# Optimization experiments

Hardware: AMD Instinct MI355X
Metric: run time of the kernel (lower is better)

## Reference

```python
import jax, jax.numpy as jnp
import numpy as np

B, L, N, H, D, TOPK = 32, 720, 512, 16, 64, 8
TEMP = 1.0


def setup_inputs() -> dict:
    key = jax.random.key(0)
    ks = jax.random.split(key, 18)
    s = lambda k, shp, fan: jax.random.normal(k, shp, jnp.float32) / np.sqrt(fan)
    return {
        'x': jax.random.normal(ks[0], (B, L, N), jnp.float32),
        'var_embed': s(ks[1], (N, H), H),
        'Wq': s(ks[2], (H, H), H), 'bq': jnp.zeros((H,), jnp.float32),
        'Wk': s(ks[3], (H, H), H), 'bk': jnp.zeros((H,), jnp.float32),
        'Wscore': s(ks[4], (N, 1), N), 'bscore': jnp.zeros((1,), jnp.float32),
        'Wc1': s(ks[5], (N, D), N), 'bc1': jnp.zeros((D,), jnp.float32),
        'Wc2': s(ks[6], (D, D), D), 'bc2': jnp.zeros((D,), jnp.float32),
        'Wcn': s(ks[7], (D, N), D), 'bcn': jnp.zeros((N,), jnp.float32),
        'Wg': s(ks[8], (2 * N, N), 2 * N), 'bg': jnp.zeros((N,), jnp.float32),
        'Wf': s(ks[9], (N, N), N), 'bf': jnp.zeros((N,), jnp.float32),
        'gamma': jnp.ones((N,), jnp.float32), 'beta': jnp.zeros((N,), jnp.float32),
    }


def _forward(x, var_embed, Wq, bq, Wk, bk, Wscore, bscore, Wc1, bc1, Wc2, bc2,
             Wcn, bcn, Wg, bg, Wf, bf, gamma, beta):
    # --- SparseVariableRouter (eval mode: no gumbel noise) ---
    Q = var_embed @ Wq + bq          # [N,H]
    K = var_embed @ Wk + bk          # [N,H]
    sim = Q @ K.T                    # [N,N] (identical across batch in torch)
    eye = jnp.eye(N, dtype=bool)
    sim = jnp.where(eye, -1e9, sim)
    topk_vals, topk_idx = jax.lax.top_k(sim, TOPK)      # [N,k]
    w = jax.nn.softmax(topk_vals / TEMP, axis=-1)        # [N,k]
    x_perm = jnp.transpose(x, (0, 2, 1))                 # [B,N,L]
    neighbors = x_perm[:, topk_idx, :]                   # [B,N,k,L] gather
    ring_out = jnp.einsum('bnkl,nk->bln', neighbors, w)  # [B,L,N]
    # --- center path ---
    attn = jax.nn.softmax(x @ Wscore + bscore, axis=1)   # [B,L,1] softmax over L
    center_raw = jnp.sum(x * attn, axis=1)               # [B,N]
    c = jax.nn.gelu(center_raw @ Wc1 + bc1, approximate=False)
    c = jax.nn.gelu(c @ Wc2 + bc2, approximate=False)
    center = c @ Wcn + bcn                               # [B,N]
    center_b = jnp.broadcast_to(center[:, None, :], (x.shape[0], x.shape[1], N))
    # --- gated fusion + residual LN ---
    gate = jax.nn.sigmoid(jnp.concatenate([ring_out, center_b], axis=-1) @ Wg + bg)
    fused = gate * ring_out + (1.0 - gate) * center_b
    fused = fused @ Wf + bf
    h = fused + x
    mu = jnp.mean(h, axis=-1, keepdims=True)
    var = jnp.var(h, axis=-1, keepdims=True)
    return (h - mu) * jax.lax.rsqrt(var + 1e-5) * gamma + beta


def reference(x, var_embed, Wq, bq, Wk, bk, Wscore, bscore, Wc1, bc1, Wc2, bc2,
              Wcn, bcn, Wg, bg, Wf, bf, gamma, beta):
    return _forward(x, var_embed, Wq, bq, Wk, bk, Wscore, bscore, Wc1, bc1,
                    Wc2, bc2, Wcn, bcn, Wg, bg, Wf, bf, gamma, beta)
```

## Files before the change

### kernel.cpp

```cpp
#include <hip/hip_runtime.h>
#include <hip/hip_bf16.h>
#include <math.h>

#define B_ 32
#define L_ 720
#define N_ 512
#define H_ 16
#define D_ 64
#define TOPK_ 8
#define M_ (B_ * L_)
#define RPB 8
#define CRCH 16
#define CRL (L_ / CRCH)
#define OROWS 64

typedef __bf16 bf16x8 __attribute__((ext_vector_type(8)));
typedef float f32x16 __attribute__((ext_vector_type(16)));

__device__ __forceinline__ void async_cp16(const __hip_bfloat16* g, __hip_bfloat16* l) {
    __builtin_amdgcn_global_load_lds(
        (const __attribute__((address_space(1))) void*)g,
        (__attribute__((address_space(3))) void*)l, 16, 0, 0);
}

__device__ __forceinline__ bf16x8 frag_ld(const __hip_bfloat16* base, int row, int j0) {
    return *(const bf16x8*)(base + row * 64 + (((j0) ^ (row & 7)) << 3));
}

__device__ __forceinline__ f32x16 fzero16() {
    f32x16 z;
    #pragma unroll
    for (int e = 0; e < 16; ++e) z[e] = 0.f;
    return z;
}

__global__ __launch_bounds__(512) void qk_kernel(
    const float* __restrict__ ve,
    const float* __restrict__ Wq, const float* __restrict__ bq,
    const float* __restrict__ Wk, const float* __restrict__ bk,
    float* __restrict__ Qm, float* __restrict__ Km)
{
    const int g = blockIdx.x * 512 + threadIdx.x;
    const int j = g >> 4, h = g & 15;
    const float* vr = ve + j * H_;
    float q = bq[h], k = bk[h];
    #pragma unroll
    for (int m = 0; m < H_; ++m) {
        const float v = vr[m];
        q += v * Wq[m * H_ + h];
        k += v * Wk[m * H_ + h];
    }
    Qm[g] = q;
    Km[g] = k;
}

__global__ __launch_bounds__(64) void topk_kernel(
    const float* __restrict__ Qm, const float* __restrict__ Km,
    float* __restrict__ w_out, int* __restrict__ idx_out)
{
    const int n = blockIdx.x;
    const int lane = threadIdx.x;

    float4 q0, q1, q2, q3;
    {
        const float4* qr = (const float4*)(Qm + n * H_);
        q0 = qr[0]; q1 = qr[1]; q2 = qr[2]; q3 = qr[3];
    }

    float sv[8]; int si[8];
    #pragma unroll
    for (int c = 0; c < 8; ++c) {
        const int j = c * 64 + lane;
        const float4* kr = (const float4*)(Km + j * H_);
        float4 k0 = kr[0], k1 = kr[1], k2 = kr[2], k3 = kr[3];
        float s = q0.x * k0.x + q0.y * k0.y + q0.z * k0.z + q0.w * k0.w
                + q1.x * k1.x + q1.y * k1.y + q1.z * k1.z + q1.w * k1.w
                + q2.x * k2.x + q2.y * k2.y + q2.z * k2.z + q2.w * k2.w
                + q3.x * k3.x + q3.y * k3.y + q3.z * k3.z + q3.w * k3.w;
        sv[c] = (j == n) ? -1e9f : s;
        si[c] = j;
    }

    float keepv[TOPK_]; int keepi[TOPK_];
    #pragma unroll
    for (int k = 0; k < TOPK_; ++k) {
        float bv = sv[0]; int bi = si[0]; int bslot = 0;
        #pragma unroll
        for (int c = 1; c < 8; ++c)
            if (sv[c] > bv || (sv[c] == bv && si[c] < bi)) { bv = sv[c]; bi = si[c]; bslot = c; }
        float v = bv; int i = bi;
        #pragma unroll
        for (int off = 32; off > 0; off >>= 1) {
            float v2 = __shfl_xor(v, off);
            int   i2 = __shfl_xor(i, off);
            if (v2 > v || (v2 == v && i2 < i)) { v = v2; i = i2; }
        }
        keepv[k] = v; keepi[k] = i;
        if (i == bi) sv[bslot] = -INFINITY;
    }

    if (lane == 0) {
        float vmax = keepv[0];
        float ev[TOPK_], esum = 0.f;
        #pragma unroll
        for (int k = 0; k < TOPK_; k++) { ev[k] = expf(keepv[k] - vmax); esum += ev[k]; }
        float inv = 1.f / esum;
        #pragma unroll
        for (int k = 0; k < TOPK_; k++) {
            w_out[n * TOPK_ + k] = ev[k] * inv;
            idx_out[n * TOPK_ + k] = keepi[k];
        }
    }
}

__global__ __launch_bounds__(512) void ring_kernel(
    const float* __restrict__ x, const float* __restrict__ w,
    const int* __restrict__ idx,
    const float* __restrict__ Wscore, const float* __restrict__ bscore,
    __hip_bfloat16* __restrict__ ring, float* __restrict__ s)
{
    __shared__ float xs[RPB][N_];
    __shared__ float wsh[N_ * TOPK_];
    __shared__ int   ish[N_ * TOPK_];
    const int t = threadIdx.x;
    const int row0 = blockIdx.x * RPB;

    for (int i = t; i < N_ * TOPK_; i += 512) { wsh[i] = w[i]; ish[i] = idx[i]; }
    {
        const float4* xg = (const float4*)(x + (size_t)row0 * N_);
        float4* xsf = (float4*)&xs[0][0];
        xsf[t] = xg[t];
        xsf[t + 512] = xg[t + 512];
    }
    __syncthreads();

    {
        const int wv = t >> 6, lane = t & 63;
        float sa = 0.f;
        #pragma unroll
        for (int i = 0; i < 8; ++i) sa += xs[wv][lane + i * 64] * Wscore[lane + i * 64];
        for (int off = 32; off > 0; off >>= 1) sa += __shfl_down(sa, off);
        if (lane == 0) s[row0 + wv] = sa + bscore[0];
    }

    float wr[TOPK_]; int ir[TOPK_];
    #pragma unroll
    for (int k = 0; k < TOPK_; ++k) { wr[k] = wsh[t * TOPK_ + k]; ir[k] = ish[t * TOPK_ + k]; }
    #pragma unroll
    for (int r = 0; r < RPB; ++r) {
        float acc = 0.f;
        #pragma unroll
        for (int k = 0; k < TOPK_; ++k) acc += wr[k] * xs[r][ir[k]];
        ring[(size_t)(row0 + r) * N_ + t] = __float2bfloat16(acc);
    }
}

__global__ __launch_bounds__(256) void attn_softmax_kernel(float* __restrict__ s)
{
    const int b = blockIdx.x;
    const int t = threadIdx.x;
    float* row = s + (size_t)b * L_;

    __shared__ float sm[4];
    __shared__ float sm2[4];

    float lmax = -1e30f;
    for (int l = t; l < L_; l += 256) lmax = fmaxf(lmax, row[l]);
    for (int off = 32; off > 0; off >>= 1) lmax = fmaxf(lmax, __shfl_down(lmax, off));
    if ((t & 63) == 0) sm[t >> 6] = lmax;
    __syncthreads();
    float gmax = fmaxf(fmaxf(sm[0], sm[1]), fmaxf(sm[2], sm[3]));

    float lsum = 0.f;
    for (int l = t; l < L_; l += 256) {
        float e = expf(row[l] - gmax);
        row[l] = e;
        lsum += e;
    }
    for (int off = 32; off > 0; off >>= 1) lsum += __shfl_down(lsum, off);
    if ((t & 63) == 0) sm2[t >> 6] = lsum;
    __syncthreads();
    float inv = 1.f / (sm2[0] + sm2[1] + sm2[2] + sm2[3]);
    for (int l = t; l < L_; l += 256) row[l] *= inv;
}

__global__ __launch_bounds__(512) void center_raw_kernel(
    const float* __restrict__ x, const float* __restrict__ attn,
    float* __restrict__ craw_p)
{
    const int b = blockIdx.x >> 4;
    const int c = blockIdx.x & 15;
    const int n = threadIdx.x;
    __shared__ float ash[CRL];
    const int l0 = c * CRL;
    if (n < CRL) ash[n] = attn[b * L_ + l0 + n];
    __syncthreads();
    const float* xb = x + ((size_t)b * L_ + l0) * N_;
    float acc = 0.f;
    #pragma unroll 3
    for (int l = 0; l < CRL; l++) acc += ash[l] * xb[(size_t)l * N_ + n];
    craw_p[(size_t)(b * CRCH + c) * N_ + n] = acc;
}

__device__ __forceinline__ float gelu_exact(float v) {
    return 0.5f * v * (1.0f + erff(v * 0.70710678118654752440f));
}

__global__ __launch_bounds__(512) void center_mlp_kernel(
    const float* __restrict__ craw_p,
    const float* __restrict__ Wc1, const float* __restrict__ bc1,
    const float* __restrict__ Wc2, const float* __restrict__ bc2,
    const float* __restrict__ Wcn, const float* __restrict__ bcn,
    float* __restrict__ center)
{
    const int b = blockIdx.x;
    const int t = threadIdx.x;
    const int col = t & 63;
    const int seg = t >> 6;
    __shared__ float cr[N_];
    __shared__ float psum[8][D_];
    __shared__ float h1[D_];
    __shared__ float h2[D_];

    {
        float acc = 0.f;
        #pragma unroll
        for (int c = 0; c < CRCH; ++c) acc += craw_p[(size_t)(b * CRCH + c) * N_ + t];
        cr[t] = acc;
    }
    __syncthreads();
    {
        float p = 0.f;
        #pragma unroll 8
        for (int m = seg * 64; m < seg * 64 + 64; ++m) p += cr[m] * Wc1[m * D_ + col];
        psum[seg][col] = p;
    }
    __syncthreads();
    if (t < D_) {
        float acc = bc1[t];
        #pragma unroll
        for (int s2 = 0; s2 < 8; ++s2) acc += psum[s2][t];
        h1[t] = gelu_exact(acc);
    }
    __syncthreads();
    if (t < D_) {
        float acc = bc2[t];
        #pragma unroll 8
        for (int j = 0; j < D_; j++) acc += h1[j] * Wc2[j * D_ + t];
        h2[t] = gelu_exact(acc);
    }
    __syncthreads();
    {
        float acc = bcn[t];
        #pragma unroll 8
        for (int j = 0; j < D_; j++) acc += h2[j] * Wcn[j * N_ + t];
        center[b * N_ + t] = acc;
    }
}

__global__ __launch_bounds__(512) void cg_kernel(
    const float* __restrict__ center, const float* __restrict__ Wg,
    const float* __restrict__ bg, float* __restrict__ cg)
{
    const int nc = blockIdx.x;
    const int b  = blockIdx.y;
    const int t  = threadIdx.x;
    const int col = nc * 64 + (t & 63);
    const int seg = t >> 6;
    __shared__ float cs[N_];
    __shared__ float psum[8][64];

    cs[t] = center[b * N_ + t];
    __syncthreads();
    {
        float p = 0.f;
        const float* wp = Wg + (size_t)(N_ + seg * 64) * N_ + col;
        #pragma unroll 8
        for (int m = 0; m < 64; ++m) { p += cs[seg * 64 + m] * wp[0]; wp += N_; }
        psum[seg][t & 63] = p;
    }
    __syncthreads();
    if (t < 64) {
        float acc = bg[nc * 64 + t];
        #pragma unroll
        for (int s2 = 0; s2 < 8; ++s2) acc += psum[s2][t];
        cg[b * N_ + nc * 64 + t] = acc;
    }
}

__global__ __launch_bounds__(256) void convert_kernel(
    const float* __restrict__ Wg, const float* __restrict__ Wf,
    __hip_bfloat16* __restrict__ WgT, __hip_bfloat16* __restrict__ WfT)
{
    const int n = blockIdx.x & 511;
    const bool isf = blockIdx.x >= 512;
    const float* src = isf ? Wf : Wg;
    __hip_bfloat16* dst = isf ? WfT : WgT;
    for (int k = threadIdx.x; k < N_; k += 256)
        dst[n * N_ + k] = __float2bfloat16(src[(size_t)k * N_ + n]);
}

#define GEMM_BODY(EPILOGUE)                                                    \
    __shared__ __hip_bfloat16 Ash[64 * 64];                                    \
    __shared__ __hip_bfloat16 Bsh[64 * 64];                                    \
    const int tid  = threadIdx.x;                                              \
    const int lane = tid & 63;                                                 \
    const int wv   = tid >> 6;                                                 \
    const int m32  = lane & 31;                                                \
    const int half = lane >> 5;                                                \
    const int wr   = wv >> 1;                                                  \
    const int wc   = wv & 1;                                                   \
    const int row0 = blockIdx.x * 64;                                          \
    const int n0   = blockIdx.y * 64;                                          \
    const int swz  = (lane & 7) ^ (lane >> 3);                                 \
    const int rln  = lane >> 3;                                                \
    f32x16 acc;                                                                \
    _Pragma("unroll") for (int e = 0; e < 16; e++) acc[e] = 0.f;               \
    for (int step = 0; step < 8; ++step) {                                     \
        const int k0 = step * 64;                                              \
        const __hip_bfloat16* Ab = A  + (size_t)row0 * N_ + k0 + swz * 8;      \
        const __hip_bfloat16* Bb = BT + (size_t)n0   * N_ + k0 + swz * 8;      \
        __syncthreads();                                                       \
        _Pragma("unroll") for (int j = 0; j < 2; ++j) {                        \
            const int r = j * 32 + wv * 8 + rln;                               \
            const int lb = (j * 256 + wv * 64) * 8;                            \
            async_cp16(Ab + (size_t)r * N_, Ash + lb);                         \
            async_cp16(Bb + (size_t)r * N_, Bsh + lb);                         \
        }                                                                      \
        __syncthreads();                                                       \
        _Pragma("unroll") for (int ks = 0; ks < 4; ++ks) {                     \
            const int j0 = ks * 2 + half;                                      \
            bf16x8 a0 = frag_ld(Ash, wr * 32 + m32, j0);                       \
            bf16x8 b0 = frag_ld(Bsh, wc * 32 + m32, j0);                       \
            acc = __builtin_amdgcn_mfma_f32_32x32x16_bf16(a0, b0, acc, 0, 0, 0); \
        }                                                                      \
    }                                                                          \
    _Pragma("unroll") for (int reg = 0; reg < 16; ++reg) {                     \
        const int rg  = row0 + wr * 32 +                                       \
                        (reg & 3) + 8 * (reg >> 2) + 4 * half;                 \
        const int col = n0 + wc * 32 + m32;                                    \
        const float aval = acc[reg];                                           \
        EPILOGUE                                                               \
    }

__global__ __launch_bounds__(256) void gemm_gate_kernel(
    const __hip_bfloat16* __restrict__ A,
    const __hip_bfloat16* __restrict__ BT,
    const float* __restrict__ cg,
    const float* __restrict__ center,
    __hip_bfloat16* __restrict__ fused)
{
    GEMM_BODY({
        const int b = rg / L_;
        const float logit = aval + cg[b * N_ + col];
        const float g = 1.f / (1.f + expf(-logit));
        const float rv = __bfloat162float(A[(size_t)rg * N_ + col]);
        const float f = g * rv + (1.f - g) * center[b * N_ + col];
        fused[(size_t)rg * N_ + col] = __float2bfloat16(f);
    })
}

__global__ __launch_bounds__(512) void gemm_out_ln_kernel(
    const __hip_bfloat16* __restrict__ A,
    const __hip_bfloat16* __restrict__ BT,
    const float* __restrict__ x,
    const float* __restrict__ bfv,
    const float* __restrict__ gamma,
    const float* __restrict__ beta,
    float* __restrict__ out)
{
    __shared__ __hip_bfloat16 Wsh[512 * 64];
    __shared__ __hip_bfloat16 Dsh[64 * 64];
    __shared__ float ps[8][2][32];
    __shared__ float pq[8][2][32];

    const int tid  = threadIdx.x;
    const int lane = tid & 63;
    const int wv8  = tid >> 6;
    const int m32  = lane & 31;
    const int half = lane >> 5;
    const int row0 = blockIdx.x * OROWS;
    const int swz  = (lane & 7) ^ (lane >> 3);
    const int rln  = lane >> 3;

    f32x16 acc[2][2];
    #pragma unroll
    for (int g = 0; g < 2; ++g)
        #pragma unroll
        for (int i = 0; i < 2; ++i) acc[g][i] = fzero16();

    for (int step = 0; step < 8; ++step) {
        const int k0 = step * 64;
        __syncthreads();
        #pragma unroll
        for (int j = 0; j < 8; ++j) {
            const int r = j * 64 + wv8 * 8 + rln;
            async_cp16(BT + (size_t)r * N_ + k0 + swz * 8,
                       Wsh + (j * 512 + wv8 * 64) * 8);
        }
        {
            const int r = wv8 * 8 + rln;
            async_cp16(A + (size_t)(row0 + r) * N_ + k0 + swz * 8,
                       Dsh + (wv8 * 64) * 8);
        }
        __syncthreads();
        #pragma unroll
        for (int ks = 0; ks < 4; ++ks) {
            const int j0 = ks * 2 + half;
            bf16x8 d0 = frag_ld(Dsh, m32, j0);
            bf16x8 d1 = frag_ld(Dsh, 32 + m32, j0);
            bf16x8 wa = frag_ld(Wsh, (wv8 * 2 + 0) * 32 + m32, j0);
            bf16x8 wb = frag_ld(Wsh, (wv8 * 2 + 1) * 32 + m32, j0);
            acc[0][0] = __builtin_amdgcn_mfma_f32_32x32x16_bf16(wa, d0, acc[0][0], 0, 0, 0);
            acc[0][1] = __builtin_amdgcn_mfma_f32_32x32x16_bf16(wb, d0, acc[0][1], 0, 0, 0);
            acc[1][0] = __builtin_amdgcn_mfma_f32_32x32x16_bf16(wa, d1, acc[1][0], 0, 0, 0);
            acc[1][1] = __builtin_amdgcn_mfma_f32_32x32x16_bf16(wb, d1, acc[1][1], 0, 0, 0);
        }
    }

    float ls[2] = {0.f, 0.f};
    float lq[2] = {0.f, 0.f};
    #pragma unroll
    for (int g = 0; g < 2; ++g) {
        const int rowg = row0 + g * 32 + m32;
        #pragma unroll
        for (int i = 0; i < 2; ++i) {
            const int ntb = (wv8 * 2 + i) * 32;
            #pragma unroll
            for (int q = 0; q < 4; ++q) {
                const int nb = ntb + 8 * q + 4 * half;
                const float4 bq = *(const float4*)(bfv + nb);
                const float4 xq = *(const float4*)(x + (size_t)rowg * N_ + nb);
                float v0 = acc[g][i][4 * q + 0] + bq.x + xq.x;
                float v1 = acc[g][i][4 * q + 1] + bq.y + xq.y;
                float v2 = acc[g][i][4 * q + 2] + bq.z + xq.z;
                float v3 = acc[g][i][4 * q + 3] + bq.w + xq.w;
                acc[g][i][4 * q + 0] = v0;
                acc[g][i][4 * q + 1] = v1;
                acc[g][i][4 * q + 2] = v2;
                acc[g][i][4 * q + 3] = v3;
                ls[g] += v0 + v1 + v2 + v3;
                lq[g] += v0 * v0 + v1 * v1 + v2 * v2 + v3 * v3;
            }
        }
    }

    #pragma unroll
    for (int g = 0; g < 2; ++g) {
        ls[g] += __shfl_xor(ls[g], 32);
        lq[g] += __shfl_xor(lq[g], 32);
    }
    if (half == 0) {
        ps[wv8][0][m32] = ls[0]; pq[wv8][0][m32] = lq[0];
        ps[wv8][1][m32] = ls[1]; pq[wv8][1][m32] = lq[1];
    }
    __syncthreads();

    #pragma unroll
    for (int g = 0; g < 2; ++g) {
        float S = 0.f, Q2 = 0.f;
        #pragma unroll
        for (int w = 0; w < 8; ++w) { S += ps[w][g][m32]; Q2 += pq[w][g][m32]; }
        const float mu  = S * (1.0f / N_);
        const float var = Q2 * (1.0f / N_) - mu * mu;
        const float inv = rsqrtf(var + 1e-5f);
        const int rowg = row0 + g * 32 + m32;
        #pragma unroll
        for (int i = 0; i < 2; ++i) {
            const int ntb = (wv8 * 2 + i) * 32;
            #pragma unroll
            for (int q = 0; q < 4; ++q) {
                const int nb = ntb + 8 * q + 4 * half;
                const float4 g4 = *(const float4*)(gamma + nb);
                const float4 b4 = *(const float4*)(beta + nb);
                float4 o;
                o.x = (acc[g][i][4 * q + 0] - mu) * inv * g4.x + b4.x;
                o.y = (acc[g][i][4 * q + 1] - mu) * inv * g4.y + b4.y;
                o.z = (acc[g][i][4 * q + 2] - mu) * inv * g4.z + b4.z;
                o.w = (acc[g][i][4 * q + 3] - mu) * inv * g4.w + b4.w;
                *(float4*)(out + (size_t)rowg * N_ + nb) = o;
            }
        }
    }
}

extern "C" void kernel_launch(void* const* d_in, const int* in_sizes, int n_in,
                              void* d_out, int out_size, void* d_ws, size_t ws_size,
                              hipStream_t stream) {
    const float* x       = (const float*)d_in[0];
    const float* ve      = (const float*)d_in[1];
    const float* Wq      = (const float*)d_in[2];
    const float* bq      = (const float*)d_in[3];
    const float* Wk      = (const float*)d_in[4];
    const float* bk      = (const float*)d_in[5];
    const float* Wscore  = (const float*)d_in[6];
    const float* bscore  = (const float*)d_in[7];
    const float* Wc1     = (const float*)d_in[8];
    const float* bc1     = (const float*)d_in[9];
    const float* Wc2     = (const float*)d_in[10];
    const float* bc2     = (const float*)d_in[11];
    const float* Wcn     = (const float*)d_in[12];
    const float* bcn     = (const float*)d_in[13];
    const float* Wg      = (const float*)d_in[14];
    const float* bg      = (const float*)d_in[15];
    const float* Wf      = (const float*)d_in[16];
    const float* bf      = (const float*)d_in[17];
    const float* gamma   = (const float*)d_in[18];
    const float* beta    = (const float*)d_in[19];
    float* out = (float*)d_out;

    char* p = (char*)d_ws;
    float* ws_w    = (float*)p; p += N_ * TOPK_ * sizeof(float);
    int*   ws_idx  = (int*)p;   p += N_ * TOPK_ * sizeof(int);
    float* ws_s    = (float*)p; p += B_ * L_ * sizeof(float);
    float* ws_crp  = (float*)p; p += B_ * CRCH * N_ * sizeof(float);
    float* ws_cent = (float*)p; p += B_ * N_ * sizeof(float);
    float* ws_cg   = (float*)p; p += B_ * N_ * sizeof(float);
    float* ws_Q    = (float*)p; p += N_ * H_ * sizeof(float);
    float* ws_K    = (float*)p; p += N_ * H_ * sizeof(float);
    __hip_bfloat16* ws_ring  = (__hip_bfloat16*)p; p += (size_t)M_ * N_ * sizeof(__hip_bfloat16);
    __hip_bfloat16* ws_fused = (__hip_bfloat16*)p; p += (size_t)M_ * N_ * sizeof(__hip_bfloat16);
    __hip_bfloat16* ws_WgT   = (__hip_bfloat16*)p; p += (size_t)N_ * N_ * sizeof(__hip_bfloat16);
    __hip_bfloat16* ws_WfT   = (__hip_bfloat16*)p; p += (size_t)N_ * N_ * sizeof(__hip_bfloat16);

    convert_kernel<<<1024, 256, 0, stream>>>(Wg, Wf, ws_WgT, ws_WfT);
    qk_kernel<<<16, 512, 0, stream>>>(ve, Wq, bq, Wk, bk, ws_Q, ws_K);
    topk_kernel<<<N_, 64, 0, stream>>>(ws_Q, ws_K, ws_w, ws_idx);
    ring_kernel<<<M_ / RPB, 512, 0, stream>>>(x, ws_w, ws_idx, Wscore, bscore,
                                              ws_ring, ws_s);
    attn_softmax_kernel<<<B_, 256, 0, stream>>>(ws_s);
    center_raw_kernel<<<B_ * CRCH, 512, 0, stream>>>(x, ws_s, ws_crp);
    center_mlp_kernel<<<B_, 512, 0, stream>>>(ws_crp, Wc1, bc1, Wc2, bc2,
                                              Wcn, bcn, ws_cent);
    cg_kernel<<<dim3(8, B_), 512, 0, stream>>>(ws_cent, Wg, bg, ws_cg);
    dim3 ggrid(M_ / 64, N_ / 64);
    gemm_gate_kernel<<<ggrid, 256, 0, stream>>>(ws_ring, ws_WgT, ws_cg,
                                                ws_cent, ws_fused);
    gemm_out_ln_kernel<<<M_ / OROWS, 512, 0, stream>>>(ws_fused, ws_WfT, x, bf,
                                                       gamma, beta, out);
}
```

Baseline: 267.1 us.

## Double-buffer LDS tiles in gate and output GEMMs to overlap loads with MFMA

Both bf16 GEMM kernels now use two LDS buffers and issue the async global-to-LDS copy for the next K-chunk before computing on the current one, so each step needs one barrier instead of two. To keep LDS within budget, the output GEMM+LayerNorm kernel halves its K-chunk to 32 and runs 16 steps, with a new 4-slot XOR swizzle. The intent is to hide global load latency behind the MFMA work. The risk is that the async loads may still not have landed when the next chunk is read, and the smaller chunks mean more barriers in the output kernel.

```diff
diff --git a/kernel.cpp b/kernel.cpp
--- a/kernel.cpp
+++ b/kernel.cpp
@@ -27,6 +27,10 @@
     return *(const bf16x8*)(base + row * 64 + (((j0) ^ (row & 7)) << 3));
 }
 
+__device__ __forceinline__ bf16x8 frag_ld4(const __hip_bfloat16* base, int row, int j0) {
+    return *(const bf16x8*)(base + row * 32 + (((j0) ^ (row & 3)) << 3));
+}
+
 __device__ __forceinline__ f32x16 fzero16() {
     f32x16 z;
     #pragma unroll
@@ -300,9 +304,17 @@
         dst[n * N_ + k] = __float2bfloat16(src[(size_t)k * N_ + n]);
 }
 
+#define GSTAGE(buf, k0)                                                        \
+    _Pragma("unroll") for (int j = 0; j < 2; ++j) {                            \
+        const int r = j * 32 + wv * 8 + rln;                                   \
+        const int lb = (j * 256 + wv * 64) * 8;                                \
+        async_cp16(Abase + (size_t)r * N_ + (k0), &Ash[buf][lb]);              \
+        async_cp16(Bbase + (size_t)r * N_ + (k0), &Bsh[buf][lb]);              \
+    }
+
 #define GEMM_BODY(EPILOGUE)                                                    \
-    __shared__ __hip_bfloat16 Ash[64 * 64];                                    \
-    __shared__ __hip_bfloat16 Bsh[64 * 64];                                    \
+    __shared__ __hip_bfloat16 Ash[2][64 * 64];                                 \
+    __shared__ __hip_bfloat16 Bsh[2][64 * 64];                                 \
     const int tid  = threadIdx.x;                                              \
     const int lane = tid & 63;                                                 \
     const int wv   = tid >> 6;                                                 \
@@ -314,26 +326,22 @@
     const int n0   = blockIdx.y * 64;                                          \
     const int swz  = (lane & 7) ^ (lane >> 3);                                 \
     const int rln  = lane >> 3;                                                \
+    const __hip_bfloat16* Abase = A  + (size_t)row0 * N_ + swz * 8;            \
+    const __hip_bfloat16* Bbase = BT + (size_t)n0   * N_ + swz * 8;            \
     f32x16 acc;                                                                \
     _Pragma("unroll") for (int e = 0; e < 16; e++) acc[e] = 0.f;               \
+    GSTAGE(0, 0)                                                               \
+    __syncthreads();                                                           \
     for (int step = 0; step < 8; ++step) {                                     \
-        const int k0 = step * 64;                                              \
-        const __hip_bfloat16* Ab = A  + (size_t)row0 * N_ + k0 + swz * 8;      \
-        const __hip_bfloat16* Bb = BT + (size_t)n0   * N_ + k0 + swz * 8;      \
-        __syncthreads();                                                       \
-        _Pragma("unroll") for (int j = 0; j < 2; ++j) {                        \
-            const int r = j * 32 + wv * 8 + rln;                               \
-            const int lb = (j * 256 + wv * 64) * 8;                            \
-            async_cp16(Ab + (size_t)r * N_, Ash + lb);                         \
-            async_cp16(Bb + (size_t)r * N_, Bsh + lb);                         \
+        const int cur = step & 1;                                              \
+        if (step < 7) { GSTAGE(cur ^ 1, (step + 1) * 64) }                     \
+        _Pragma("unroll") for (int ks = 0; ks < 4; ++ks) {                     \
+            const int j0 = ks * 2 + half;                                      \
+            bf16x8 a0 = frag_ld(Ash[cur], wr * 32 + m32, j0);                  \
+            bf16x8 b0 = frag_ld(Bsh[cur], wc * 32 + m32, j0);                  \
+            acc = __builtin_amdgcn_mfma_f32_32x32x16_bf16(a0, b0, acc, 0, 0, 0); \
         }                                                                      \
         __syncthreads();                                                       \
-        _Pragma("unroll") for (int ks = 0; ks < 4; ++ks) {                     \
-            const int j0 = ks * 2 + half;                                      \
-            bf16x8 a0 = frag_ld(Ash, wr * 32 + m32, j0);                       \
-            bf16x8 b0 = frag_ld(Bsh, wc * 32 + m32, j0);                       \
-            acc = __builtin_amdgcn_mfma_f32_32x32x16_bf16(a0, b0, acc, 0, 0, 0); \
-        }                                                                      \
     }                                                                          \
     _Pragma("unroll") for (int reg = 0; reg < 16; ++reg) {                     \
         const int rg  = row0 + wr * 32 +                                       \
@@ -360,6 +368,18 @@
     })
 }
 
+#define OSTAGE(buf, k0)                                                        \
+    _Pragma("unroll") for (int j = 0; j < 4; ++j) {                            \
+        const int r = j * 128 + (tid >> 2);                                    \
+        async_cp16(BT + (size_t)r * N_ + (k0) + wslot * 8,                     \
+                   &Wsh[buf][j * 4096 + wv8 * 512]);                           \
+    }                                                                          \
+    if (wv8 < 4) {                                                             \
+        const int r = wv8 * 16 + (lane >> 2);                                  \
+        async_cp16(A + (size_t)(row0 + r) * N_ + (k0) + dslot * 8,             \
+                   &Dsh[buf][wv8 * 512]);                                      \
+    }
+
 __global__ __launch_bounds__(512) void gemm_out_ln_kernel(
     const __hip_bfloat16* __restrict__ A,
     const __hip_bfloat16* __restrict__ BT,
@@ -369,8 +389,8 @@
     const float* __restrict__ beta,
     float* __restrict__ out)
 {
-    __shared__ __hip_bfloat16 Wsh[512 * 64];
-    __shared__ __hip_bfloat16 Dsh[64 * 64];
+    __shared__ __hip_bfloat16 Wsh[2][512 * 32];
+    __shared__ __hip_bfloat16 Dsh[2][64 * 32];
     __shared__ float ps[8][2][32];
     __shared__ float pq[8][2][32];
 
@@ -380,8 +400,8 @@
     const int m32  = lane & 31;
     const int half = lane >> 5;
     const int row0 = blockIdx.x * OROWS;
-    const int swz  = (lane & 7) ^ (lane >> 3);
-    const int rln  = lane >> 3;
+    const int wslot = (tid & 3) ^ ((tid >> 2) & 3);
+    const int dslot = (lane & 3) ^ ((lane >> 2) & 3);
 
     f32x16 acc[2][2];
     #pragma unroll
@@ -389,33 +409,24 @@
         #pragma unroll
         for (int i = 0; i < 2; ++i) acc[g][i] = fzero16();
 
-    for (int step = 0; step < 8; ++step) {
-        const int k0 = step * 64;
-        __syncthreads();
-        #pragma unroll
-        for (int j = 0; j < 8; ++j) {
-            const int r = j * 64 + wv8 * 8 + rln;
-            async_cp16(BT + (size_t)r * N_ + k0 + swz * 8,
-                       Wsh + (j * 512 + wv8 * 64) * 8);
-        }
-        {
-            const int r = wv8 * 8 + rln;
-            async_cp16(A + (size_t)(row0 + r) * N_ + k0 + swz * 8,
-                       Dsh + (wv8 * 64) * 8);
-        }
-        __syncthreads();
-        #pragma unroll
-        for (int ks = 0; ks < 4; ++ks) {
+    OSTAGE(0, 0)
+    __syncthreads();
+    for (int c = 0; c < 16; ++c) {
+        const int cur = c & 1;
+        if (c < 15) { OSTAGE(cur ^ 1, (c + 1) * 32) }
+        #pragma unroll
+        for (int ks = 0; ks < 2; ++ks) {
             const int j0 = ks * 2 + half;
-            bf16x8 d0 = frag_ld(Dsh, m32, j0);
-            bf16x8 d1 = frag_ld(Dsh, 32 + m32, j0);
-            bf16x8 wa = frag_ld(Wsh, (wv8 * 2 + 0) * 32 + m32, j0);
-            bf16x8 wb = frag_ld(Wsh, (wv8 * 2 + 1) * 32 + m32, j0);
+            bf16x8 d0 = frag_ld4(Dsh[cur], m32, j0);
+            bf16x8 d1 = frag_ld4(Dsh[cur], 32 + m32, j0);
+            bf16x8 wa = frag_ld4(Wsh[cur], (wv8 * 2 + 0) * 32 + m32, j0);
+            bf16x8 wb = frag_ld4(Wsh[cur], (wv8 * 2 + 1) * 32 + m32, j0);
             acc[0][0] = __builtin_amdgcn_mfma_f32_32x32x16_bf16(wa, d0, acc[0][0], 0, 0, 0);
             acc[0][1] = __builtin_amdgcn_mfma_f32_32x32x16_bf16(wb, d0, acc[0][1], 0, 0, 0);
             acc[1][0] = __builtin_amdgcn_mfma_f32_32x32x16_bf16(wa, d1, acc[1][0], 0, 0, 0);
             acc[1][1] = __builtin_amdgcn_mfma_f32_32x32x16_bf16(wb, d1, acc[1][1], 0, 0, 0);
         }
+        __syncthreads();
     }
 
     float ls[2] = {0.f, 0.f};
```

Result: slower. 274.5 us (+2.8%).

## Fuse small prep, softmax and center-gate kernels to cut launch count

Applied to the files above, without the earlier changes.

Merges the weight transpose/convert and QK projection into one prep kernel, folds the attention softmax into center_raw (each block recomputes max/sum over the row), and folds the center-gate matvec into center_mlp. This removes three kernel launches and their serialization gaps. In exchange the softmax reduction is redundantly recomputed by 16 blocks per batch, and the cg matvec now runs with only 32 blocks doing a serial 512-long loop each, which may lengthen that stage. The gate GEMM epilogue also replaces a per-element division with a compare.

```diff
diff --git a/kernel.cpp b/kernel.cpp
--- a/kernel.cpp
+++ b/kernel.cpp
@@ -34,24 +34,34 @@
     return z;
 }
 
-__global__ __launch_bounds__(512) void qk_kernel(
+__global__ __launch_bounds__(512) void prep_kernel(
+    const float* __restrict__ Wg, const float* __restrict__ Wf,
+    __hip_bfloat16* __restrict__ WgT, __hip_bfloat16* __restrict__ WfT,
     const float* __restrict__ ve,
     const float* __restrict__ Wq, const float* __restrict__ bq,
     const float* __restrict__ Wk, const float* __restrict__ bk,
     float* __restrict__ Qm, float* __restrict__ Km)
 {
-    const int g = blockIdx.x * 512 + threadIdx.x;
-    const int j = g >> 4, h = g & 15;
-    const float* vr = ve + j * H_;
-    float q = bq[h], k = bk[h];
-    #pragma unroll
-    for (int m = 0; m < H_; ++m) {
-        const float v = vr[m];
-        q += v * Wq[m * H_ + h];
-        k += v * Wk[m * H_ + h];
-    }
-    Qm[g] = q;
-    Km[g] = k;
+    const int bx = blockIdx.x;
+    if (bx < 512) {
+        const int n = bx;
+        const int k = threadIdx.x;
+        WgT[n * N_ + k] = __float2bfloat16(Wg[(size_t)k * N_ + n]);
+        WfT[n * N_ + k] = __float2bfloat16(Wf[(size_t)k * N_ + n]);
+    } else {
+        const int g = (bx - 512) * 512 + threadIdx.x;
+        const int j = g >> 4, h = g & 15;
+        const float* vr = ve + j * H_;
+        float q = bq[h], k = bk[h];
+        #pragma unroll
+        for (int m = 0; m < H_; ++m) {
+            const float v = vr[m];
+            q += v * Wq[m * H_ + h];
+            k += v * Wk[m * H_ + h];
+        }
+        Qm[g] = q;
+        Km[g] = k;
+    }
 }
 
 __global__ __launch_bounds__(64) void topk_kernel(
@@ -155,46 +165,41 @@
     }
 }
 
-__global__ __launch_bounds__(256) void attn_softmax_kernel(float* __restrict__ s)
-{
-    const int b = blockIdx.x;
-    const int t = threadIdx.x;
-    float* row = s + (size_t)b * L_;
-
-    __shared__ float sm[4];
-    __shared__ float sm2[4];
-
-    float lmax = -1e30f;
-    for (int l = t; l < L_; l += 256) lmax = fmaxf(lmax, row[l]);
-    for (int off = 32; off > 0; off >>= 1) lmax = fmaxf(lmax, __shfl_down(lmax, off));
-    if ((t & 63) == 0) sm[t >> 6] = lmax;
-    __syncthreads();
-    float gmax = fmaxf(fmaxf(sm[0], sm[1]), fmaxf(sm[2], sm[3]));
-
-    float lsum = 0.f;
-    for (int l = t; l < L_; l += 256) {
-        float e = expf(row[l] - gmax);
-        row[l] = e;
-        lsum += e;
-    }
-    for (int off = 32; off > 0; off >>= 1) lsum += __shfl_down(lsum, off);
-    if ((t & 63) == 0) sm2[t >> 6] = lsum;
-    __syncthreads();
-    float inv = 1.f / (sm2[0] + sm2[1] + sm2[2] + sm2[3]);
-    for (int l = t; l < L_; l += 256) row[l] *= inv;
-}
-
 __global__ __launch_bounds__(512) void center_raw_kernel(
-    const float* __restrict__ x, const float* __restrict__ attn,
+    const float* __restrict__ x, const float* __restrict__ s,
     float* __restrict__ craw_p)
 {
     const int b = blockIdx.x >> 4;
     const int c = blockIdx.x & 15;
     const int n = threadIdx.x;
+    __shared__ float red[8];
     __shared__ float ash[CRL];
+    const float* srow = s + (size_t)b * L_;
+
+    float lmax = -1e30f;
+    for (int l = n; l < L_; l += 512) lmax = fmaxf(lmax, srow[l]);
+    for (int off = 32; off > 0; off >>= 1) lmax = fmaxf(lmax, __shfl_down(lmax, off));
+    if ((n & 63) == 0) red[n >> 6] = lmax;
+    __syncthreads();
+    float gmax = red[0];
+    #pragma unroll
+    for (int w = 1; w < 8; ++w) gmax = fmaxf(gmax, red[w]);
+    __syncthreads();
+
+    float lsum = 0.f;
+    for (int l = n; l < L_; l += 512) lsum += expf(srow[l] - gmax);
+    for (int off = 32; off > 0; off >>= 1) lsum += __shfl_down(lsum, off);
+    if ((n & 63) == 0) red[n >> 6] = lsum;
+    __syncthreads();
+    float tsum = 0.f;
+    #pragma unroll
+    for (int w = 0; w < 8; ++w) tsum += red[w];
+    const float inv = 1.f / tsum;
+
     const int l0 = c * CRL;
-    if (n < CRL) ash[n] = attn[b * L_ + l0 + n];
-    __syncthreads();
+    if (n < CRL) ash[n] = expf(srow[l0 + n] - gmax) * inv;
+    __syncthreads();
+
     const float* xb = x + ((size_t)b * L_ + l0) * N_;
     float acc = 0.f;
     #pragma unroll 3
@@ -211,7 +216,8 @@
     const float* __restrict__ Wc1, const float* __restrict__ bc1,
     const float* __restrict__ Wc2, const float* __restrict__ bc2,
     const float* __restrict__ Wcn, const float* __restrict__ bcn,
-    float* __restrict__ center)
+    const float* __restrict__ Wg,  const float* __restrict__ bg,
+    float* __restrict__ center, float* __restrict__ cg)
 {
     const int b = blockIdx.x;
     const int t = threadIdx.x;
@@ -250,54 +256,24 @@
         h2[t] = gelu_exact(acc);
     }
     __syncthreads();
+    float centv;
     {
         float acc = bcn[t];
         #pragma unroll 8
         for (int j = 0; j < D_; j++) acc += h2[j] * Wcn[j * N_ + t];
+        centv = acc;
         center[b * N_ + t] = acc;
     }
-}
-
-__global__ __launch_bounds__(512) void cg_kernel(
-    const float* __restrict__ center, const float* __restrict__ Wg,
-    const float* __restrict__ bg, float* __restrict__ cg)
-{
-    const int nc = blockIdx.x;
-    const int b  = blockIdx.y;
-    const int t  = threadIdx.x;
-    const int col = nc * 64 + (t & 63);
-    const int seg = t >> 6;
-    __shared__ float cs[N_];
-    __shared__ float psum[8][64];
-
-    cs[t] = center[b * N_ + t];
-    __syncthreads();
-    {
-        float p = 0.f;
-        const float* wp = Wg + (size_t)(N_ + seg * 64) * N_ + col;
+    __syncthreads();
+    cr[t] = centv;
+    __syncthreads();
+    {
+        float acc = bg[t];
+        const float* wp = Wg + (size_t)N_ * N_ + t;
         #pragma unroll 8
-        for (int m = 0; m < 64; ++m) { p += cs[seg * 64 + m] * wp[0]; wp += N_; }
-        psum[seg][t & 63] = p;
-    }
-    __syncthreads();
-    if (t < 64) {
-        float acc = bg[nc * 64 + t];
-        #pragma unroll
-        for (int s2 = 0; s2 < 8; ++s2) acc += psum[s2][t];
-        cg[b * N_ + nc * 64 + t] = acc;
-    }
-}
-
-__global__ __launch_bounds__(256) void convert_kernel(
-    const float* __restrict__ Wg, const float* __restrict__ Wf,
-    __hip_bfloat16* __restrict__ WgT, __hip_bfloat16* __restrict__ WfT)
-{
-    const int n = blockIdx.x & 511;
-    const bool isf = blockIdx.x >= 512;
-    const float* src = isf ? Wf : Wg;
-    __hip_bfloat16* dst = isf ? WfT : WgT;
-    for (int k = threadIdx.x; k < N_; k += 256)
-        dst[n * N_ + k] = __float2bfloat16(src[(size_t)k * N_ + n]);
+        for (int m = 0; m < N_; ++m) { acc += cr[m] * wp[0]; wp += N_; }
+        cg[b * N_ + t] = acc;
+    }
 }
 
 #define GEMM_BODY(EPILOGUE)                                                    \
@@ -351,7 +327,8 @@
     __hip_bfloat16* __restrict__ fused)
 {
     GEMM_BODY({
-        const int b = rg / L_;
+        const int bbase = row0 / L_;
+        const int b = (rg >= (bbase + 1) * L_) ? bbase + 1 : bbase;
         const float logit = aval + cg[b * N_ + col];
         const float g = 1.f / (1.f + expf(-logit));
         const float rv = __bfloat162float(A[(size_t)rg * N_ + col]);
@@ -523,16 +500,14 @@
     __hip_bfloat16* ws_WgT   = (__hip_bfloat16*)p; p += (size_t)N_ * N_ * sizeof(__hip_bfloat16);
     __hip_bfloat16* ws_WfT   = (__hip_bfloat16*)p; p += (size_t)N_ * N_ * sizeof(__hip_bfloat16);
 
-    convert_kernel<<<1024, 256, 0, stream>>>(Wg, Wf, ws_WgT, ws_WfT);
-    qk_kernel<<<16, 512, 0, stream>>>(ve, Wq, bq, Wk, bk, ws_Q, ws_K);
+    prep_kernel<<<528, 512, 0, stream>>>(Wg, Wf, ws_WgT, ws_WfT,
+                                         ve, Wq, bq, Wk, bk, ws_Q, ws_K);
     topk_kernel<<<N_, 64, 0, stream>>>(ws_Q, ws_K, ws_w, ws_idx);
     ring_kernel<<<M_ / RPB, 512, 0, stream>>>(x, ws_w, ws_idx, Wscore, bscore,
                                               ws_ring, ws_s);
-    attn_softmax_kernel<<<B_, 256, 0, stream>>>(ws_s);
     center_raw_kernel<<<B_ * CRCH, 512, 0, stream>>>(x, ws_s, ws_crp);
     center_mlp_kernel<<<B_, 512, 0, stream>>>(ws_crp, Wc1, bc1, Wc2, bc2,
-                                              Wcn, bcn, ws_cent);
-    cg_kernel<<<dim3(8, B_), 512, 0, stream>>>(ws_cent, Wg, bg, ws_cg);
+                                              Wcn, bcn, Wg, bg, ws_cent, ws_cg);
     dim3 ggrid(M_ / 64, N_ / 64);
     gemm_gate_kernel<<<ggrid, 256, 0, stream>>>(ws_ring, ws_WgT, ws_cg,
                                                 ws_cent, ws_fused);
```

Result: slower. 277.9 us (+4.0%).
